# Kernel optimization log

Measured on AMD Instinct MI355X. Metric: run time of the kernel, lower is better.

## Reference

```python
import jax, jax.numpy as jnp
import numpy as np

B, C, H, W = 4, 256, 64, 64

def setup_inputs() -> dict:
    key = jax.random.key(0)
    ks = jax.random.split(key, 6)
    inv = 1.0 / np.sqrt(C)
    return {
        "feature": jax.random.normal(ks[0], (B, C, H, W), dtype=jnp.float32),
        "flow": jax.random.normal(ks[1], (B, 2, H, W), dtype=jnp.float32),
        "q_w": jax.random.uniform(ks[2], (C, C), dtype=jnp.float32, minval=-inv, maxval=inv),
        "q_b": jax.random.uniform(ks[3], (C,), dtype=jnp.float32, minval=-inv, maxval=inv),
        "k_w": jax.random.uniform(ks[4], (C, C), dtype=jnp.float32, minval=-inv, maxval=inv),
        "k_b": jax.random.uniform(ks[5], (C,), dtype=jnp.float32, minval=-inv, maxval=inv),
    }

def reference(feature, flow, q_w, q_b, k_w, k_b):
    b, c, h, w = feature.shape
    # [b,c,h,w] -> [b, h*w, c] tokens
    tok = feature.reshape(b, c, h * w).transpose(0, 2, 1)
    v = flow.reshape(b, 2, h * w).transpose(0, 2, 1)       # [b, hw, 2]
    q = jnp.einsum('bnc,dc->bnd', tok, q_w) + q_b           # Linear(c,c)
    k = jnp.einsum('bnc,dc->bnd', tok, k_w) + k_b
    scale = 1.0 / jnp.sqrt(jnp.asarray(c, dtype=q.dtype))
    scores = jnp.einsum('bld,bsd->bls', q, k) * scale       # [b, hw, hw]
    attn = jax.nn.softmax(scores, axis=-1)                  # dropout_p=0 -> no-op
    out = jnp.einsum('bls,bsv->blv', attn, v)               # [b, hw, 2]
    return out.reshape(b, h, w, 2).transpose(0, 3, 1, 2)    # [b, 2, h, w]
```

## Files before the change

### kernel.cpp

```cpp
#include <hip/hip_runtime.h>
#include <math.h>

#define BB 4
#define CC 256
#define HWN 4096
#define NTOK 16384
#define SCQ 0.09016844136f

typedef __attribute__((ext_vector_type(8))) short short8;
typedef __attribute__((ext_vector_type(4))) float f32x4;
typedef unsigned short ushort_t;

__device__ __forceinline__ ushort_t f2bf(float f) {
    unsigned int u = __float_as_uint(f);
    unsigned int r = (u + 0x7FFFu + ((u >> 16) & 1u)) >> 16;
    return (ushort_t)r;
}
__device__ __forceinline__ unsigned int pack2(float a, float b) {
    return (unsigned int)f2bf(a) | ((unsigned int)f2bf(b) << 16);
}

__global__ __launch_bounds__(256, 2) void proj_kernel(
    const float* __restrict__ feature,
    const float* __restrict__ q_w, const float* __restrict__ k_w,
    const float* __restrict__ q_bias, const float* __restrict__ k_bias,
    ushort_t* __restrict__ qb, ushort_t* __restrict__ kb,
    float* __restrict__ zbuf)
{
    int gid = blockIdx.x * 256 + threadIdx.x;
    if (gid < 3 * NTOK) zbuf[gid] = 0.f;

    int tt = blockIdx.x & 63;
    int b  = blockIdx.x >> 6;
    int tok0 = tt * 64;

    int t = threadIdx.x, w = t >> 6, lane = t & 63;
    int n16 = lane & 15, quad = lane >> 4;

    __shared__ float    lsA[64][69];
    __shared__ ushort_t lsB[64][264];

    const float* F = feature + (size_t)(b * CC) * HWN;

    int cl = t >> 2, tg = (t & 3) * 16;
    int tokw = t >> 2, c16 = (t & 3) * 16;

    for (int ch = 0; ch < 4; ch++) {
        const float* src = F + (size_t)(ch * 64 + cl) * HWN + tok0 + tg;
        *(float4*)&lsA[cl][tg]      = *(const float4*)(src);
        *(float4*)&lsA[cl][tg + 4]  = *(const float4*)(src + 4);
        *(float4*)&lsA[cl][tg + 8]  = *(const float4*)(src + 8);
        *(float4*)&lsA[cl][tg + 12] = *(const float4*)(src + 12);
        __syncthreads();
        #pragma unroll
        for (int jj = 0; jj < 8; jj++)
            *(unsigned int*)&lsB[tokw][ch * 64 + c16 + 2 * jj] =
                pack2(lsA[c16 + 2 * jj][tokw], lsA[c16 + 2 * jj + 1][tokw]);
        __syncthreads();
    }

    int dw0 = w * 64;
    #pragma unroll
    for (int dsub = 0; dsub < 4; dsub++) {
        int d0 = dw0 + dsub * 16;
        f32x4 accq[4], acck[4];
        #pragma unroll
        for (int i = 0; i < 4; i++) {
            accq[i] = (f32x4){0.f, 0.f, 0.f, 0.f};
            acck[i] = (f32x4){0.f, 0.f, 0.f, 0.f};
        }
        #pragma unroll
        for (int kc = 0; kc < 8; kc++) {
            size_t off = (size_t)(d0 + n16) * CC + kc * 32 + quad * 8;
            float4 a0 = *(const float4*)&q_w[off];
            float4 a1 = *(const float4*)&q_w[off + 4];
            short8 aq, ak;
            aq[0] = (short)f2bf(a0.x * SCQ); aq[1] = (short)f2bf(a0.y * SCQ);
            aq[2] = (short)f2bf(a0.z * SCQ); aq[3] = (short)f2bf(a0.w * SCQ);
            aq[4] = (short)f2bf(a1.x * SCQ); aq[5] = (short)f2bf(a1.y * SCQ);
            aq[6] = (short)f2bf(a1.z * SCQ); aq[7] = (short)f2bf(a1.w * SCQ);
            a0 = *(const float4*)&k_w[off];
            a1 = *(const float4*)&k_w[off + 4];
            ak[0] = (short)f2bf(a0.x); ak[1] = (short)f2bf(a0.y);
            ak[2] = (short)f2bf(a0.z); ak[3] = (short)f2bf(a0.w);
            ak[4] = (short)f2bf(a1.x); ak[5] = (short)f2bf(a1.y);
            ak[6] = (short)f2bf(a1.z); ak[7] = (short)f2bf(a1.w);
            #pragma unroll
            for (int tokt = 0; tokt < 4; tokt++) {
                short8 bf = *(const short8*)&lsB[tokt * 16 + n16][kc * 32 + quad * 8];
                accq[tokt] = __builtin_amdgcn_mfma_f32_16x16x32_bf16(aq, bf, accq[tokt], 0, 0, 0);
                acck[tokt] = __builtin_amdgcn_mfma_f32_16x16x32_bf16(ak, bf, acck[tokt], 0, 0, 0);
            }
        }
        float bqv[4], bkv[4];
        #pragma unroll
        for (int r = 0; r < 4; r++) {
            bqv[r] = q_bias[d0 + quad * 4 + r] * SCQ;
            bkv[r] = k_bias[d0 + quad * 4 + r];
        }
        #pragma unroll
        for (int tokt = 0; tokt < 4; tokt++) {
            size_t row = (size_t)(b * HWN + tok0 + tokt * 16 + n16) * CC + d0 + quad * 4;
            ushort4 oq, ok;
            oq.x = f2bf(accq[tokt][0] + bqv[0]); oq.y = f2bf(accq[tokt][1] + bqv[1]);
            oq.z = f2bf(accq[tokt][2] + bqv[2]); oq.w = f2bf(accq[tokt][3] + bqv[3]);
            ok.x = f2bf(acck[tokt][0] + bkv[0]); ok.y = f2bf(acck[tokt][1] + bkv[1]);
            ok.z = f2bf(acck[tokt][2] + bkv[2]); ok.w = f2bf(acck[tokt][3] + bkv[3]);
            *(ushort4*)&qb[row] = oq;
            *(ushort4*)&kb[row] = ok;
        }
    }
}

__global__ __launch_bounds__(256, 2) void attn_kernel(
    const ushort_t* __restrict__ qb, const ushort_t* __restrict__ kb,
    const float* __restrict__ flow,
    float* __restrict__ den_g, float* __restrict__ nx_g, float* __restrict__ ny_g)
{
    int id = blockIdx.x;
    int qt = id & 15; id >>= 4;
    int sr = id & 7;  id >>= 3;
    int b = id;

    int t = threadIdx.x;
    int w = t >> 6, lane = t & 63;
    int n16 = lane & 15, quad = lane >> 4;

    int q0 = qt * 256 + w * 64;
    int s_beg = sr * 512;

    const ushort_t* Qb = qb + (size_t)b * HWN * CC;
    const ushort_t* Kb = kb + (size_t)b * HWN * CC;

    __shared__ __align__(16) ushort_t lk[2][8192];
    __shared__ float lflow[1024];

    const float* fx = flow + (size_t)b * 2 * HWN;
    const float* fy = fx + HWN;
    lflow[t]        = fx[s_beg + t];
    lflow[t + 256]  = fx[s_beg + t + 256];
    lflow[t + 512]  = fy[s_beg + t];
    lflow[t + 768]  = fy[s_beg + t + 256];

    short8 qf[4][8];
    #pragma unroll
    for (int tq = 0; tq < 4; tq++)
        #pragma unroll
        for (int c = 0; c < 8; c++)
            qf[tq][c] = *(const short8*)&Qb[(size_t)(q0 + tq * 16 + n16) * CC
                                            + c * 32 + quad * 8];

    int srcoff[4];
    #pragma unroll
    for (int i = 0; i < 4; i++) {
        int G = i * 256 + t;
        int r = G >> 5, j = G & 31;
        srcoff[i] = (r * 32 + (j ^ r)) * 16;
    }
    int p16[8];
    #pragma unroll
    for (int c = 0; c < 8; c++)
        p16[c] = (((c * 4 + quad) ^ n16) & 31) * 16;

    float den[4][4], nxa[4][4], nya[4][4];
    #pragma unroll
    for (int tq = 0; tq < 4; tq++)
        #pragma unroll
        for (int r = 0; r < 4; r++) { den[tq][r] = 0.f; nxa[tq][r] = 0.f; nya[tq][r] = 0.f; }

    {
        const char* gsrc = (const char*)(Kb + (size_t)s_beg * CC);
        char* ldst = (char*)lk[0] + t * 16;
        #pragma unroll
        for (int i = 0; i < 4; i++)
            __builtin_amdgcn_global_load_lds(
                (const __attribute__((address_space(1))) unsigned int*)(gsrc + srcoff[i]),
                (__attribute__((address_space(3))) unsigned int*)(ldst + i * 4096),
                16, 0, 0);
    }

    for (int st = 0; st < 16; st++) {
        __syncthreads();
        if (st + 1 < 16) {
            const char* gsrc = (const char*)(Kb + (size_t)(s_beg + (st + 1) * 32) * CC);
            char* ldst = (char*)lk[(st + 1) & 1] + t * 16;
            #pragma unroll
            for (int i = 0; i < 4; i++)
                __builtin_amdgcn_global_load_lds(
                    (const __attribute__((address_space(1))) unsigned int*)(gsrc + srcoff[i]),
                    (__attribute__((address_space(3))) unsigned int*)(ldst + i * 4096),
                    16, 0, 0);
        }
        const char* base = (const char*)lk[st & 1];

        #pragma unroll
        for (int bt = 0; bt < 2; bt++) {
            int rbase = (bt * 16 + n16) * 512;
            int x16   = bt ? 256 : 0;
            f32x4 a0 = {0.f, 0.f, 0.f, 0.f};
            f32x4 a1 = {0.f, 0.f, 0.f, 0.f};
            f32x4 a2 = {0.f, 0.f, 0.f, 0.f};
            f32x4 a3 = {0.f, 0.f, 0.f, 0.f};
            #pragma unroll
            for (int c = 0; c < 8; c++) {
                short8 kf = *(const short8*)(base + rbase + (p16[c] ^ x16));
                a0 = __builtin_amdgcn_mfma_f32_16x16x32_bf16(qf[0][c], kf, a0, 0, 0, 0);
                a1 = __builtin_amdgcn_mfma_f32_16x16x32_bf16(qf[1][c], kf, a1, 0, 0, 0);
                a2 = __builtin_amdgcn_mfma_f32_16x16x32_bf16(qf[2][c], kf, a2, 0, 0, 0);
                a3 = __builtin_amdgcn_mfma_f32_16x16x32_bf16(qf[3][c], kf, a3, 0, 0, 0);
            }
            int sidx = st * 32 + bt * 16 + n16;
            float vx = lflow[sidx];
            float vy = lflow[512 + sidx];
            #pragma unroll
            for (int r = 0; r < 4; r++) {
                float p0 = exp2f(a0[r]);
                float p1 = exp2f(a1[r]);
                float p2 = exp2f(a2[r]);
                float p3 = exp2f(a3[r]);
                den[0][r] += p0; den[1][r] += p1; den[2][r] += p2; den[3][r] += p3;
                nxa[0][r] = fmaf(p0, vx, nxa[0][r]); nxa[1][r] = fmaf(p1, vx, nxa[1][r]);
                nxa[2][r] = fmaf(p2, vx, nxa[2][r]); nxa[3][r] = fmaf(p3, vx, nxa[3][r]);
                nya[0][r] = fmaf(p0, vy, nya[0][r]); nya[1][r] = fmaf(p1, vy, nya[1][r]);
                nya[2][r] = fmaf(p2, vy, nya[2][r]); nya[3][r] = fmaf(p3, vy, nya[3][r]);
            }
        }
    }

    #pragma unroll
    for (int tq = 0; tq < 4; tq++)
        #pragma unroll
        for (int r = 0; r < 4; r++) {
            #pragma unroll
            for (int off = 8; off >= 1; off >>= 1) {
                den[tq][r] += __shfl_down(den[tq][r], off, 16);
                nxa[tq][r] += __shfl_down(nxa[tq][r], off, 16);
                nya[tq][r] += __shfl_down(nya[tq][r], off, 16);
            }
        }
    if (n16 == 0) {
        #pragma unroll
        for (int tq = 0; tq < 4; tq++)
            #pragma unroll
            for (int r = 0; r < 4; r++) {
                int qrow = q0 + tq * 16 + quad * 4 + r;
                int gi = b * HWN + qrow;
                atomicAdd(&den_g[gi], den[tq][r]);
                atomicAdd(&nx_g[gi],  nxa[tq][r]);
                atomicAdd(&ny_g[gi],  nya[tq][r]);
            }
    }
}

__global__ __launch_bounds__(256) void finalize_kernel(
    const float* __restrict__ den_g, const float* __restrict__ nx_g,
    const float* __restrict__ ny_g, float* __restrict__ out)
{
    int idx = blockIdx.x * 256 + threadIdx.x;
    int b = idx >> 12, n = idx & 4095;
    float inv = 1.0f / den_g[idx];
    out[(size_t)b * 2 * HWN + n]       = nx_g[idx] * inv;
    out[(size_t)b * 2 * HWN + HWN + n] = ny_g[idx] * inv;
}

extern "C" void kernel_launch(void* const* d_in, const int* in_sizes, int n_in,
                              void* d_out, int out_size, void* d_ws, size_t ws_size,
                              hipStream_t stream) {
    const float* feature = (const float*)d_in[0];
    const float* flow    = (const float*)d_in[1];
    const float* q_w     = (const float*)d_in[2];
    const float* q_b     = (const float*)d_in[3];
    const float* k_w     = (const float*)d_in[4];
    const float* k_b     = (const float*)d_in[5];
    float* out = (float*)d_out;

    ushort_t* qbuf = (ushort_t*)d_ws;
    ushort_t* kbuf = qbuf + (size_t)NTOK * CC;
    float* den = (float*)(kbuf + (size_t)NTOK * CC);
    float* nx  = den + NTOK;
    float* ny  = nx + NTOK;

    proj_kernel<<<256, 256, 0, stream>>>(feature, q_w, k_w, q_b, k_b,
                                         qbuf, kbuf, den);
    attn_kernel<<<512, 256, 0, stream>>>(qbuf, kbuf, flow, den, nx, ny);
    finalize_kernel<<<64, 256, 0, stream>>>(den, nx, ny, out);
}
```

Baseline: 141.5 us.

## Pre-convert weights to bf16, split projection grid, remap attention blocks, pack softmax accumulation

A new prep kernel converts the Q/K weights to bf16 once and zeroes the accumulators, so the projection kernel no longer repeats that conversion in every block. The projection grid doubles to 512 blocks by splitting output channels in half, which raises parallelism at the cost of transposing the feature tile twice. The attention kernel remaps block indices so consecutive blocks cover different source ranges and batches, and it packs the exp/FMA accumulation into 2-wide float vectors to allow packed FP32 instructions. The change also adds a fourth kernel launch and a workspace region for the bf16 weights.

```diff
diff --git a/kernel.cpp b/kernel.cpp
--- a/kernel.cpp
+++ b/kernel.cpp
@@ -9,6 +9,7 @@
 
 typedef __attribute__((ext_vector_type(8))) short short8;
 typedef __attribute__((ext_vector_type(4))) float f32x4;
+typedef __attribute__((ext_vector_type(2))) float f32x2;
 typedef unsigned short ushort_t;
 
 __device__ __forceinline__ ushort_t f2bf(float f) {
@@ -20,18 +21,34 @@
     return (unsigned int)f2bf(a) | ((unsigned int)f2bf(b) << 16);
 }
 
+__global__ __launch_bounds__(256) void wprep_kernel(
+    const float* __restrict__ q_w, const float* __restrict__ k_w,
+    ushort_t* __restrict__ qwb, ushort_t* __restrict__ kwb,
+    float* __restrict__ zbuf)
+{
+    int t = blockIdx.x * 256 + threadIdx.x;
+    float4 q4 = *(const float4*)&q_w[(size_t)t * 4];
+    float4 k4 = *(const float4*)&k_w[(size_t)t * 4];
+    unsigned long long qo = (unsigned long long)pack2(q4.x * SCQ, q4.y * SCQ)
+                          | ((unsigned long long)pack2(q4.z * SCQ, q4.w * SCQ) << 32);
+    unsigned long long ko = (unsigned long long)pack2(k4.x, k4.y)
+                          | ((unsigned long long)pack2(k4.z, k4.w) << 32);
+    *(unsigned long long*)&qwb[(size_t)t * 4] = qo;
+    *(unsigned long long*)&kwb[(size_t)t * 4] = ko;
+    zbuf[t] = 0.f; zbuf[t + NTOK] = 0.f; zbuf[t + 2 * NTOK] = 0.f;
+}
+
 __global__ __launch_bounds__(256, 2) void proj_kernel(
     const float* __restrict__ feature,
-    const float* __restrict__ q_w, const float* __restrict__ k_w,
+    const ushort_t* __restrict__ qwb, const ushort_t* __restrict__ kwb,
     const float* __restrict__ q_bias, const float* __restrict__ k_bias,
-    ushort_t* __restrict__ qb, ushort_t* __restrict__ kb,
-    float* __restrict__ zbuf)
+    ushort_t* __restrict__ qb, ushort_t* __restrict__ kb)
 {
-    int gid = blockIdx.x * 256 + threadIdx.x;
-    if (gid < 3 * NTOK) zbuf[gid] = 0.f;
-
-    int tt = blockIdx.x & 63;
-    int b  = blockIdx.x >> 6;
+    int id = blockIdx.x;
+    int dh = id >> 8;
+    id &= 255;
+    int tt = id & 63;
+    int b  = id >> 6;
     int tok0 = tt * 64;
 
     int t = threadIdx.x, w = t >> 6, lane = t & 63;
@@ -59,9 +76,9 @@
         __syncthreads();
     }
 
-    int dw0 = w * 64;
-    #pragma unroll
-    for (int dsub = 0; dsub < 4; dsub++) {
+    int dw0 = dh * 128 + w * 32;
+    #pragma unroll
+    for (int dsub = 0; dsub < 2; dsub++) {
         int d0 = dw0 + dsub * 16;
         f32x4 accq[4], acck[4];
         #pragma unroll
@@ -72,19 +89,8 @@
         #pragma unroll
         for (int kc = 0; kc < 8; kc++) {
             size_t off = (size_t)(d0 + n16) * CC + kc * 32 + quad * 8;
-            float4 a0 = *(const float4*)&q_w[off];
-            float4 a1 = *(const float4*)&q_w[off + 4];
-            short8 aq, ak;
-            aq[0] = (short)f2bf(a0.x * SCQ); aq[1] = (short)f2bf(a0.y * SCQ);
-            aq[2] = (short)f2bf(a0.z * SCQ); aq[3] = (short)f2bf(a0.w * SCQ);
-            aq[4] = (short)f2bf(a1.x * SCQ); aq[5] = (short)f2bf(a1.y * SCQ);
-            aq[6] = (short)f2bf(a1.z * SCQ); aq[7] = (short)f2bf(a1.w * SCQ);
-            a0 = *(const float4*)&k_w[off];
-            a1 = *(const float4*)&k_w[off + 4];
-            ak[0] = (short)f2bf(a0.x); ak[1] = (short)f2bf(a0.y);
-            ak[2] = (short)f2bf(a0.z); ak[3] = (short)f2bf(a0.w);
-            ak[4] = (short)f2bf(a1.x); ak[5] = (short)f2bf(a1.y);
-            ak[6] = (short)f2bf(a1.z); ak[7] = (short)f2bf(a1.w);
+            short8 aq = *(const short8*)&qwb[off];
+            short8 ak = *(const short8*)&kwb[off];
             #pragma unroll
             for (int tokt = 0; tokt < 4; tokt++) {
                 short8 bf = *(const short8*)&lsB[tokt * 16 + n16][kc * 32 + quad * 8];
@@ -117,7 +123,7 @@
     const float* __restrict__ flow,
     float* __restrict__ den_g, float* __restrict__ nx_g, float* __restrict__ ny_g)
 {
-    int id = blockIdx.x;
+    int id = (blockIdx.x & 7) * 64 + (blockIdx.x >> 3);
     int qt = id & 15; id >>= 4;
     int sr = id & 7;  id >>= 3;
     int b = id;
@@ -162,11 +168,15 @@
     for (int c = 0; c < 8; c++)
         p16[c] = (((c * 4 + quad) ^ n16) & 31) * 16;
 
-    float den[4][4], nxa[4][4], nya[4][4];
+    f32x2 den[4][2], nxa[4][2], nya[4][2];
     #pragma unroll
     for (int tq = 0; tq < 4; tq++)
         #pragma unroll
-        for (int r = 0; r < 4; r++) { den[tq][r] = 0.f; nxa[tq][r] = 0.f; nya[tq][r] = 0.f; }
+        for (int j = 0; j < 2; j++) {
+            den[tq][j] = (f32x2){0.f, 0.f};
+            nxa[tq][j] = (f32x2){0.f, 0.f};
+            nya[tq][j] = (f32x2){0.f, 0.f};
+        }
 
     {
         const char* gsrc = (const char*)(Kb + (size_t)s_beg * CC);
@@ -212,17 +222,19 @@
             int sidx = st * 32 + bt * 16 + n16;
             float vx = lflow[sidx];
             float vy = lflow[512 + sidx];
-            #pragma unroll
-            for (int r = 0; r < 4; r++) {
-                float p0 = exp2f(a0[r]);
-                float p1 = exp2f(a1[r]);
-                float p2 = exp2f(a2[r]);
-                float p3 = exp2f(a3[r]);
-                den[0][r] += p0; den[1][r] += p1; den[2][r] += p2; den[3][r] += p3;
-                nxa[0][r] = fmaf(p0, vx, nxa[0][r]); nxa[1][r] = fmaf(p1, vx, nxa[1][r]);
-                nxa[2][r] = fmaf(p2, vx, nxa[2][r]); nxa[3][r] = fmaf(p3, vx, nxa[3][r]);
-                nya[0][r] = fmaf(p0, vy, nya[0][r]); nya[1][r] = fmaf(p1, vy, nya[1][r]);
-                nya[2][r] = fmaf(p2, vy, nya[2][r]); nya[3][r] = fmaf(p3, vy, nya[3][r]);
+            f32x2 vx2 = (f32x2){vx, vx};
+            f32x2 vy2 = (f32x2){vy, vy};
+            #pragma unroll
+            for (int tq = 0; tq < 4; tq++) {
+                f32x4 a = (tq == 0) ? a0 : (tq == 1) ? a1 : (tq == 2) ? a2 : a3;
+                f32x2 p0 = (f32x2){exp2f(a[0]), exp2f(a[1])};
+                f32x2 p1 = (f32x2){exp2f(a[2]), exp2f(a[3])};
+                den[tq][0] += p0;
+                den[tq][1] += p1;
+                nxa[tq][0] = __builtin_elementwise_fma(p0, vx2, nxa[tq][0]);
+                nxa[tq][1] = __builtin_elementwise_fma(p1, vx2, nxa[tq][1]);
+                nya[tq][0] = __builtin_elementwise_fma(p0, vy2, nya[tq][0]);
+                nya[tq][1] = __builtin_elementwise_fma(p1, vy2, nya[tq][1]);
             }
         }
     }
@@ -230,26 +242,27 @@
     #pragma unroll
     for (int tq = 0; tq < 4; tq++)
         #pragma unroll
-        for (int r = 0; r < 4; r++) {
-            #pragma unroll
-            for (int off = 8; off >= 1; off >>= 1) {
-                den[tq][r] += __shfl_down(den[tq][r], off, 16);
-                nxa[tq][r] += __shfl_down(nxa[tq][r], off, 16);
-                nya[tq][r] += __shfl_down(nya[tq][r], off, 16);
+        for (int j = 0; j < 2; j++)
+            #pragma unroll
+            for (int e = 0; e < 2; e++) {
+                float dv = den[tq][j][e];
+                float xv = nxa[tq][j][e];
+                float yv = nya[tq][j][e];
+                #pragma unroll
+                for (int off = 8; off >= 1; off >>= 1) {
+                    dv += __shfl_down(dv, off, 16);
+                    xv += __shfl_down(xv, off, 16);
+                    yv += __shfl_down(yv, off, 16);
+                }
+                if (n16 == 0) {
+                    int r = j * 2 + e;
+                    int qrow = q0 + tq * 16 + quad * 4 + r;
+                    int gi = b * HWN + qrow;
+                    atomicAdd(&den_g[gi], dv);
+                    atomicAdd(&nx_g[gi],  xv);
+                    atomicAdd(&ny_g[gi],  yv);
+                }
             }
-        }
-    if (n16 == 0) {
-        #pragma unroll
-        for (int tq = 0; tq < 4; tq++)
-            #pragma unroll
-            for (int r = 0; r < 4; r++) {
-                int qrow = q0 + tq * 16 + quad * 4 + r;
-                int gi = b * HWN + qrow;
-                atomicAdd(&den_g[gi], den[tq][r]);
-                atomicAdd(&nx_g[gi],  nxa[tq][r]);
-                atomicAdd(&ny_g[gi],  nya[tq][r]);
-            }
-    }
 }
 
 __global__ __launch_bounds__(256) void finalize_kernel(
@@ -279,9 +292,11 @@
     float* den = (float*)(kbuf + (size_t)NTOK * CC);
     float* nx  = den + NTOK;
     float* ny  = nx + NTOK;
-
-    proj_kernel<<<256, 256, 0, stream>>>(feature, q_w, k_w, q_b, k_b,
-                                         qbuf, kbuf, den);
+    ushort_t* qwb = (ushort_t*)(ny + NTOK);
+    ushort_t* kwb = qwb + (size_t)CC * CC;
+
+    wprep_kernel<<<64, 256, 0, stream>>>(q_w, k_w, qwb, kwb, den);
+    proj_kernel<<<512, 256, 0, stream>>>(feature, qwb, kwb, q_b, k_b, qbuf, kbuf);
     attn_kernel<<<512, 256, 0, stream>>>(qbuf, kbuf, flow, den, nx, ny);
     finalize_kernel<<<64, 256, 0, stream>>>(den, nx, ny, out);
 }
```

After: 140.0 us. Within noise of the previous version (-1.1%).
